# Kernel optimization log

Hardware: AMD Instinct MI355X
Metric: run time of the kernel (lower is better)

Reference implementation:

```python
import jax, jax.numpy as jnp
import numpy as np

N_H = 16
N_KV = 4
D_K = 128
ROPE_BASE = 10000.0


def _rope(t, cos, sin):
    # t: [B, T, H, d_k]; cos/sin: [1, T, 1, d_k//2]
    te, to = t[..., 0::2], t[..., 1::2]
    oe = te * cos - to * sin
    oo = te * sin + to * cos
    return jnp.stack([oe, oo], axis=-1).reshape(t.shape)


def setup_inputs() -> dict:
    key = jax.random.key(0)
    ks = jax.random.split(key, 5)
    B, T, d = 4, 2048, 2048
    s = 0.02
    return {
        "x": jax.random.normal(ks[0], (B, T, d), jnp.float32),
        "Wq": jax.random.normal(ks[1], (d, d), jnp.float32) * s,
        "Wk": jax.random.normal(ks[2], (d, N_KV * D_K), jnp.float32) * s,
        "Wv": jax.random.normal(ks[3], (d, N_KV * D_K), jnp.float32) * s,
        "Wp": jax.random.normal(ks[4], (d, d), jnp.float32) * s,
        "bp": jnp.zeros((d,), jnp.float32),
    }


def reference(x, Wq, Wk, Wv, Wp, bp):
    B, T, C = x.shape
    g = N_H // N_KV  # group size

    q = (x @ Wq).reshape(B, T, N_H, D_K)
    k = (x @ Wk).reshape(B, T, N_KV, D_K)
    v = (x @ Wv).reshape(B, T, N_KV, D_K)

    # RoPE frequencies (constants)
    theta = ROPE_BASE ** (-2.0 * jnp.arange(0, D_K, 2, dtype=jnp.float32) / D_K)
    freq = jnp.arange(T, dtype=jnp.float32)[:, None] * theta[None, :]  # [T, d_k//2]
    cos = jnp.cos(freq)[None, :, None, :]
    sin = jnp.sin(freq)[None, :, None, :]
    q = _rope(q, cos, sin)
    k = _rope(k, cos, sin)

    # GQA: group q heads by shared kv head (equiv to repeat_interleave on kv)
    q = q.reshape(B, T, N_KV, g, D_K).transpose(0, 2, 3, 1, 4)  # [B,n_kv,g,T,d_k]
    k = k.transpose(0, 2, 1, 3)  # [B,n_kv,T,d_k]
    v = v.transpose(0, 2, 1, 3)

    scores = jnp.einsum('bngqd,bnkd->bngqk', q, k) * (D_K ** -0.5)
    causal = jnp.tril(jnp.ones((T, T), bool))
    scores = jnp.where(causal, scores, -jnp.inf)
    attn = jax.nn.softmax(scores, axis=-1)
    out = jnp.einsum('bngqk,bnkd->bngqd', attn, v)  # [B,n_kv,g,T,d_k]
    out = out.transpose(0, 3, 1, 2, 4).reshape(B, T, C)
    return out @ Wp + bp
```

## Files before the change

kernel.cpp:

```cpp
#include <hip/hip_runtime.h>
#include <hip/hip_bf16.h>
#include <math.h>

typedef __bf16 bf16_t;
typedef __bf16 bf16x8 __attribute__((ext_vector_type(8)));
typedef __bf16 bf16x4 __attribute__((ext_vector_type(4)));
typedef float f32x4 __attribute__((ext_vector_type(4)));
typedef float f32x16 __attribute__((ext_vector_type(16)));
typedef unsigned int u32;

#define MFMA16 __builtin_amdgcn_mfma_f32_16x16x32_bf16
#define MFMA32 __builtin_amdgcn_mfma_f32_32x32x16_bf16

static __device__ __forceinline__ u32 pkbf(float a, float b) {
  union { bf16_t h[2]; u32 u; } z;
  z.h[0] = (bf16_t)a; z.h[1] = (bf16_t)b;
  return z.u;
}

static __device__ __forceinline__ void gload16(const bf16_t* g, bf16_t* l) {
  __builtin_amdgcn_global_load_lds(
      (const __attribute__((address_space(1))) void*)g,
      (__attribute__((address_space(3))) void*)l, 16, 0, 0);
}

__global__ void k_f32_to_bf16(const float* __restrict__ in, bf16_t* __restrict__ out, long n) {
  long i = ((long)blockIdx.x * blockDim.x + threadIdx.x) * 4;
  long stride = (long)gridDim.x * blockDim.x * 4;
  for (; i < n; i += stride) {
    const float4 v = *(const float4*)(in + i);
    bf16x4 o; o[0] = (bf16_t)v.x; o[1] = (bf16_t)v.y; o[2] = (bf16_t)v.z; o[3] = (bf16_t)v.w;
    *(bf16x4*)(out + i) = o;
  }
}

__global__ void k_transpose_bf16(const float* __restrict__ W, bf16_t* __restrict__ WT,
                                 int K, int N) {
  __shared__ float tile[32][33];
  int n0 = blockIdx.x * 32, k0 = blockIdx.y * 32;
  int tx = threadIdx.x & 31, ty = threadIdx.x >> 5;
#pragma unroll
  for (int i = 0; i < 4; i++)
    tile[ty + i * 8][tx] = W[(size_t)(k0 + ty + i * 8) * N + n0 + tx];
  __syncthreads();
#pragma unroll
  for (int i = 0; i < 4; i++) {
    int n = ty + i * 8;
    WT[(size_t)(n0 + n) * K + k0 + tx] = (bf16_t)tile[tx][n];
  }
}

__global__ void k_build_vt(const bf16_t* __restrict__ qkv, bf16_t* __restrict__ VT) {
  __shared__ bf16_t tile[32][33];
  int t0 = blockIdx.x * 32, c0 = blockIdx.y * 32, b = blockIdx.z;
  int tx = threadIdx.x & 31, ty = threadIdx.x >> 5;
  const bf16_t* src = qkv + (size_t)b * 2048 * 3072 + 2560;
#pragma unroll
  for (int i = 0; i < 4; i++)
    tile[ty + i * 8][tx] = src[(size_t)(t0 + ty + i * 8) * 3072 + c0 + tx];
  __syncthreads();
  bf16_t* dst = VT + (size_t)b * 512 * 2048;
#pragma unroll
  for (int i = 0; i < 4; i++)
    dst[(size_t)(c0 + ty + i * 8) * 2048 + t0 + tx] = tile[tx][ty + i * 8];
}

__global__ void k_rope(bf16_t* __restrict__ qkv) {
  int idx = blockIdx.x * blockDim.x + threadIdx.x;
  if (idx >= 8192 * 1280) return;
  int r = idx / 1280, p = idx - r * 1280;
  int t = r & 2047;
  int i = p & 63;
  float theta = exp2f(-(float)i * 0.41524101186092029f);
  float f = (float)t * theta;
  float s, c;
  sincosf(f, &s, &c);
  bf16_t* a = qkv + (size_t)r * 3072 + p * 2;
  float e = (float)a[0], o = (float)a[1];
  a[0] = (bf16_t)(e * c - o * s);
  a[1] = (bf16_t)(e * s + o * c);
}

template <bool F32OUT>
__global__ __launch_bounds__(256, 3) void k_gemm_bt(
    const bf16_t* __restrict__ A, const bf16_t* __restrict__ BT,
    bf16_t* __restrict__ Cb, float* __restrict__ Cf,
    const float* __restrict__ bias, int M, int N, int K, int nwg) {
  __shared__ bf16_t sA[128 * 64];
  __shared__ bf16_t sB[128 * 64];
  int nbn = N >> 7;
  int orig = (int)blockIdx.x;
  int swz = (orig & 7) * (nwg >> 3) + (orig >> 3);
  int bm = swz / nbn, bn = swz % nbn;
  int tid = threadIdx.x;
  int lane = tid & 63, wid = tid >> 6;
  int wm = (wid >> 1) << 6, wn = (wid & 1) << 6;
  int lr = lane & 15, lq = lane >> 4;
  f32x4 acc[4][4] = {};

  int srow = wid * 32 + (lane >> 3);
  int scol = (lane & 7) * 8;
  const bf16_t* Ag = A + (size_t)(bm * 128 + srow) * K + scol;
  const bf16_t* Bg = BT + (size_t)(bn * 128 + srow) * K + scol;
  bf16_t* Al = &sA[(wid * 32) * 64];
  bf16_t* Bl = &sB[(wid * 32) * 64];

  for (int k0 = 0; k0 < K; k0 += 64) {
#pragma unroll
    for (int i = 0; i < 4; i++) {
      gload16(Ag + (size_t)i * 8 * K + k0, Al + i * 8 * 64);
      gload16(Bg + (size_t)i * 8 * K + k0, Bl + i * 8 * 64);
    }
    __syncthreads();
#pragma unroll
    for (int kc = 0; kc < 2; kc++) {
      bf16x8 af[4], bfr[4];
#pragma unroll
      for (int m = 0; m < 4; m++)
        af[m] = *(const bf16x8*)&sA[(wm + m * 16 + lr) * 64 + kc * 32 + lq * 8];
#pragma unroll
      for (int n = 0; n < 4; n++)
        bfr[n] = *(const bf16x8*)&sB[(wn + n * 16 + lr) * 64 + kc * 32 + lq * 8];
#pragma unroll
      for (int m = 0; m < 4; m++)
#pragma unroll
        for (int n = 0; n < 4; n++)
          acc[m][n] = MFMA16(af[m], bfr[n], acc[m][n], 0, 0, 0);
    }
    __syncthreads();
  }
#pragma unroll
  for (int m = 0; m < 4; m++) {
    int row0 = bm * 128 + wm + m * 16 + lq * 4;
#pragma unroll
    for (int n = 0; n < 4; n++) {
      int col = bn * 128 + wn + n * 16 + lr;
#pragma unroll
      for (int r = 0; r < 4; r++) {
        if constexpr (F32OUT)
          Cf[(size_t)(row0 + r) * N + col] = acc[m][n][r] + bias[col];
        else
          Cb[(size_t)(row0 + r) * N + col] = (bf16_t)acc[m][n][r];
      }
    }
  }
}

__global__ __launch_bounds__(256, 2) void k_attn(const bf16_t* __restrict__ qkv,
                                                 const bf16_t* __restrict__ VT,
                                                 bf16_t* __restrict__ out) {
  __shared__ bf16_t sK[64 * 128];
  __shared__ bf16_t sVT[128 * 64];
  int bid = blockIdx.x;
  int g = bid >> 6;
  int qt = (g & 1) ? (g >> 1) : (15 - (g >> 1));
  int bh = bid & 63;
  int h = bh & 15, b = bh >> 4;
  int kvh = h >> 2;
  const size_t RS = 3072;
  const bf16_t* Qb = qkv + (size_t)b * 2048 * RS + h * 128;
  const bf16_t* Kb = qkv + (size_t)b * 2048 * RS + 2048 + kvh * 128;
  const bf16_t* Vt = VT + (size_t)(b * 4 + kvh) * 128 * 2048;
  int q0 = qt * 128;
  int tid = threadIdx.x, lane = tid & 63, wid = tid >> 6;
  int l31 = lane & 31, hi = lane >> 5;
  int qw = q0 + wid * 32;

  bf16x8 qf[8];
  {
    const bf16_t* qrow = Qb + (size_t)(qw + l31) * RS + hi * 8;
#pragma unroll
    for (int dc = 0; dc < 8; dc++)
      qf[dc] = *(const bf16x8*)(qrow + dc * 16);
  }

  f32x16 oT[4] = {};
  float m_r = -INFINITY, l_r = 0.f;
  const float SC = 0.08838834764831845f * 1.4426950408889634f;

  int k_row = tid >> 4, k_seg = tid & 15;
  int vd = tid >> 3, vk = (tid & 7) * 8;

  bf16x8 kreg[4], vreg[4];
  auto issue = [&](int k0) {
#pragma unroll
    for (int ps = 0; ps < 4; ps++)
      kreg[ps] = *(const bf16x8*)(Kb + (size_t)(k0 + k_row + ps * 16) * RS + k_seg * 8);
#pragma unroll
    for (int ps = 0; ps < 4; ps++)
      vreg[ps] = *(const bf16x8*)(Vt + (size_t)(vd + ps * 32) * 2048 + k0 + vk);
  };

  int ntiles = 2 * qt + 2;
  issue(0);
  for (int kt = 0; kt < ntiles; kt++) {
    int k0 = kt * 64;
#pragma unroll
    for (int ps = 0; ps < 4; ps++) {
      int row = k_row + ps * 16;
      int off = row * 256 + ((k_seg * 16) ^ ((row & 7) << 4));
      *(bf16x8*)((char*)sK + off) = kreg[ps];
    }
#pragma unroll
    for (int ps = 0; ps < 4; ps++) {
      int d = vd + ps * 32;
      int off = d * 128 + ((vk * 2) ^ ((d & 7) << 4));
      *(bf16x8*)((char*)sVT + off) = vreg[ps];
    }
    __syncthreads();
    if (kt + 1 < ntiles) issue(k0 + 64);

    if (k0 <= qw + 31) {
      f32x16 sa0 = {}, sa1 = {};
      __builtin_amdgcn_s_setprio(1);
#pragma unroll
      for (int dc = 0; dc < 8; dc++) {
        int cb = (dc * 32 + hi * 16) ^ ((l31 & 7) << 4);
        bf16x8 kf0 = *(const bf16x8*)((const char*)sK + l31 * 256 + cb);
        bf16x8 kf1 = *(const bf16x8*)((const char*)sK + (32 + l31) * 256 + cb);
        sa0 = MFMA32(kf0, qf[dc], sa0, 0, 0, 0);
        sa1 = MFMA32(kf1, qf[dc], sa1, 0, 0, 0);
      }
      __builtin_amdgcn_s_setprio(0);
      float p[2][16];
      int qg = qw + l31;
      if (k0 + 63 <= qw) {
#pragma unroll
        for (int r = 0; r < 16; r++) { p[0][r] = sa0[r]; p[1][r] = sa1[r]; }
      } else {
#pragma unroll
        for (int nf = 0; nf < 2; nf++)
#pragma unroll
          for (int r = 0; r < 16; r++) {
            int kg = k0 + nf * 32 + (r & 3) + 8 * (r >> 2) + 4 * hi;
            p[nf][r] = (kg <= qg) ? (nf ? sa1[r] : sa0[r]) : -INFINITY;
          }
      }
      float mx[16];
#pragma unroll
      for (int r = 0; r < 16; r++) mx[r] = fmaxf(p[0][r], p[1][r]);
#pragma unroll
      for (int s = 8; s >= 1; s >>= 1)
#pragma unroll
        for (int r = 0; r < 8; r++)
          if (r < s) mx[r] = fmaxf(mx[r], mx[r + s]);
      float pm = mx[0] * SC;
      pm = fmaxf(pm, __shfl_xor(pm, 32));
      bool skip = __all(pm <= m_r + 8.f);
      float mn = skip ? m_r : fmaxf(m_r, pm);
      float alpha = skip ? 1.f : exp2f(m_r - mn);
      m_r = mn;
      float nm = -m_r;
#pragma unroll
      for (int nf = 0; nf < 2; nf++)
#pragma unroll
        for (int r = 0; r < 16; r++)
          p[nf][r] = exp2f(fmaf(p[nf][r], SC, nm));
      float sm[16];
#pragma unroll
      for (int r = 0; r < 16; r++) sm[r] = p[0][r] + p[1][r];
#pragma unroll
      for (int s = 8; s >= 1; s >>= 1)
#pragma unroll
        for (int r = 0; r < 8; r++)
          if (r < s) sm[r] += sm[r + s];
      float rs = sm[0] + __shfl_xor(sm[0], 32);
      l_r = l_r * alpha + rs;
      if (!skip) {
#pragma unroll
        for (int c = 0; c < 4; c++)
#pragma unroll
          for (int r = 0; r < 16; r++) oT[c][r] *= alpha;
      }
#pragma unroll
      for (int nf = 0; nf < 2; nf++) {
        u32 Qk[4][2];
#pragma unroll
        for (int gg = 0; gg < 4; gg++) {
          Qk[gg][0] = pkbf(p[nf][4 * gg + 0], p[nf][4 * gg + 1]);
          Qk[gg][1] = pkbf(p[nf][4 * gg + 2], p[nf][4 * gg + 3]);
        }
#pragma unroll
        for (int kc = 0; kc < 2; kc++) {
          u32 x0 = __shfl_xor(Qk[2 * kc + 1 - hi][0], 32);
          u32 x1 = __shfl_xor(Qk[2 * kc + 1 - hi][1], 32);
          u32 o0 = Qk[2 * kc + hi][0], o1 = Qk[2 * kc + hi][1];
          union { u32 w[4]; bf16x8 v; } pf;
          pf.w[0] = hi ? x0 : o0;
          pf.w[1] = hi ? x1 : o1;
          pf.w[2] = hi ? o0 : x0;
          pf.w[3] = hi ? o1 : x1;
          int slot = nf * 2 + kc;
          int vb = (slot * 32 + hi * 16) ^ ((l31 & 7) << 4);
          __builtin_amdgcn_s_setprio(1);
#pragma unroll
          for (int c = 0; c < 4; c++) {
            bf16x8 vf = *(const bf16x8*)((const char*)sVT + (c * 32 + l31) * 128 + vb);
            oT[c] = MFMA32(vf, pf.v, oT[c], 0, 0, 0);
          }
          __builtin_amdgcn_s_setprio(0);
        }
      }
    }
    __syncthreads();
  }
  float inv = 1.f / l_r;
  size_t row = (size_t)b * 2048 + qw + l31;
#pragma unroll
  for (int c = 0; c < 4; c++)
#pragma unroll
    for (int rr = 0; rr < 4; rr++) {
      bf16x4 o4;
#pragma unroll
      for (int j = 0; j < 4; j++) o4[j] = (bf16_t)(oT[c][rr * 4 + j] * inv);
      *(bf16x4*)(out + row * 2048 + h * 128 + c * 32 + rr * 8 + hi * 4) = o4;
    }
}

extern "C" void kernel_launch(void* const* d_in, const int* in_sizes, int n_in,
                              void* d_out, int out_size, void* d_ws, size_t ws_size,
                              hipStream_t stream) {
  const float* x = (const float*)d_in[0];
  const float* Wq = (const float*)d_in[1];
  const float* Wk = (const float*)d_in[2];
  const float* Wv = (const float*)d_in[3];
  const float* Wp = (const float*)d_in[4];
  const float* bp = (const float*)d_in[5];
  float* out = (float*)d_out;

  bf16_t* ws = (bf16_t*)d_ws;
  bf16_t* xb = ws;
  bf16_t* qkv = ws + 16777216;
  bf16_t* WqkvT = ws + 16777216 + 25165824;
  bf16_t* WpT = WqkvT + 6291456;
  bf16_t* VT = WqkvT;

  k_f32_to_bf16<<<2048, 256, 0, stream>>>(x, xb, 16777216L);
  k_transpose_bf16<<<dim3(64, 64), 256, 0, stream>>>(Wq, WqkvT, 2048, 2048);
  k_transpose_bf16<<<dim3(16, 64), 256, 0, stream>>>(Wk, WqkvT + (size_t)2048 * 2048, 2048, 512);
  k_transpose_bf16<<<dim3(16, 64), 256, 0, stream>>>(Wv, WqkvT + (size_t)2560 * 2048, 2048, 512);
  k_transpose_bf16<<<dim3(64, 64), 256, 0, stream>>>(Wp, WpT, 2048, 2048);

  k_gemm_bt<false><<<64 * 24, 256, 0, stream>>>(xb, WqkvT, qkv, nullptr, nullptr, 8192, 3072, 2048, 64 * 24);
  k_rope<<<40960, 256, 0, stream>>>(qkv);
  k_build_vt<<<dim3(64, 16, 4), 256, 0, stream>>>(qkv, VT);
  k_attn<<<1024, 256, 0, stream>>>(qkv, VT, xb);
  k_gemm_bt<true><<<64 * 16, 256, 0, stream>>>(xb, WpT, nullptr, out, bp, 8192, 2048, 2048, 64 * 16);
}
```

Before: 435.8 us.

## Rewrite GEMM as 256x256 double-buffered swizzled tiles, pad attention V-transpose LDS

```diff
diff --git a/kernel.cpp b/kernel.cpp
--- a/kernel.cpp
+++ b/kernel.cpp
@@ -82,59 +82,123 @@
 }
 
 template <bool F32OUT>
-__global__ __launch_bounds__(256, 3) void k_gemm_bt(
+__global__ __launch_bounds__(512, 2) void k_gemm_bt(
     const bf16_t* __restrict__ A, const bf16_t* __restrict__ BT,
     bf16_t* __restrict__ Cb, float* __restrict__ Cf,
     const float* __restrict__ bias, int M, int N, int K, int nwg) {
-  __shared__ bf16_t sA[128 * 64];
-  __shared__ bf16_t sB[128 * 64];
-  int nbn = N >> 7;
+  __shared__ bf16_t smem[65536];
+  const int nbn = N >> 8;
   int orig = (int)blockIdx.x;
   int swz = (orig & 7) * (nwg >> 3) + (orig >> 3);
   int bm = swz / nbn, bn = swz % nbn;
-  int tid = threadIdx.x;
-  int lane = tid & 63, wid = tid >> 6;
-  int wm = (wid >> 1) << 6, wn = (wid & 1) << 6;
-  int lr = lane & 15, lq = lane >> 4;
-  f32x4 acc[4][4] = {};
-
-  int srow = wid * 32 + (lane >> 3);
-  int scol = (lane & 7) * 8;
-  const bf16_t* Ag = A + (size_t)(bm * 128 + srow) * K + scol;
-  const bf16_t* Bg = BT + (size_t)(bn * 128 + srow) * K + scol;
-  bf16_t* Al = &sA[(wid * 32) * 64];
-  bf16_t* Bl = &sB[(wid * 32) * 64];
-
-  for (int k0 = 0; k0 < K; k0 += 64) {
+  const int tid = threadIdx.x;
+  const int lane = tid & 63, wid = tid >> 6;
+  const int wm = (wid >> 2) << 7;
+  const int wn = (wid & 3) << 6;
+  const int lr = lane & 15, lq = lane >> 4;
+  f32x4 acc[8][4] = {};
+
+  const int rl = tid >> 3;
+  const int ss = (tid & 7) ^ (rl & 7);
+  const bf16_t* gA = A + (size_t)(bm * 256 + rl) * K + ss * 8;
+  const bf16_t* gB = BT + (size_t)(bn * 256 + rl) * K + ss * 8;
+  const int lo = wid * 512;
+
+  const int nt = K >> 6;
+  {
+    bf16_t* sA0 = smem;
+    bf16_t* sB0 = smem + 16384;
 #pragma unroll
     for (int i = 0; i < 4; i++) {
-      gload16(Ag + (size_t)i * 8 * K + k0, Al + i * 8 * 64);
-      gload16(Bg + (size_t)i * 8 * K + k0, Bl + i * 8 * 64);
-    }
-    __syncthreads();
-#pragma unroll
-    for (int kc = 0; kc < 2; kc++) {
-      bf16x8 af[4], bfr[4];
-#pragma unroll
-      for (int m = 0; m < 4; m++)
-        af[m] = *(const bf16x8*)&sA[(wm + m * 16 + lr) * 64 + kc * 32 + lq * 8];
-#pragma unroll
-      for (int n = 0; n < 4; n++)
-        bfr[n] = *(const bf16x8*)&sB[(wn + n * 16 + lr) * 64 + kc * 32 + lq * 8];
-#pragma unroll
-      for (int m = 0; m < 4; m++)
+      gload16(gA + (size_t)i * 64 * K, sA0 + i * 4096 + lo);
+      gload16(gB + (size_t)i * 64 * K, sB0 + i * 4096 + lo);
+    }
+  }
+  asm volatile("s_waitcnt vmcnt(0)" ::: "memory");
+  __syncthreads();
+
+  for (int t = 0; t < nt; ++t) {
+    bf16_t* sAc = smem + (t & 1) * 32768;
+    bf16_t* sBc = sAc + 16384;
+    bf16_t* sAn = smem + ((t & 1) ^ 1) * 32768;
+    bf16_t* sBn = sAn + 16384;
+    const int k1 = (t + 1) << 6;
+    bf16x8 breg[4][2];
+#pragma unroll
+    for (int n = 0; n < 4; n++)
+#pragma unroll
+      for (int kk = 0; kk < 2; kk++) {
+        int R = wn + n * 16 + lr;
+        int u = (kk * 4 + lq) ^ (R & 7);
+        breg[n][kk] = *(const bf16x8*)&sBc[R * 64 + u * 8];
+      }
+    {
+      bf16x8 areg[2][2];
+#pragma unroll
+      for (int ml = 0; ml < 2; ml++)
+#pragma unroll
+        for (int kk = 0; kk < 2; kk++) {
+          int R = wm + ml * 16 + lr;
+          int u = (kk * 4 + lq) ^ (R & 7);
+          areg[ml][kk] = *(const bf16x8*)&sAc[R * 64 + u * 8];
+        }
+      if (t + 1 < nt) {
+#pragma unroll
+        for (int i = 0; i < 4; i++) {
+          gload16(gA + (size_t)i * 64 * K + k1, sAn + i * 4096 + lo);
+          gload16(gB + (size_t)i * 64 * K + k1, sBn + i * 4096 + lo);
+        }
+      }
+      __builtin_amdgcn_s_barrier();
+      asm volatile("s_waitcnt lgkmcnt(0)" ::: "memory");
+      __builtin_amdgcn_sched_barrier(0);
+      __builtin_amdgcn_s_setprio(1);
+#pragma unroll
+      for (int ml = 0; ml < 2; ml++)
 #pragma unroll
         for (int n = 0; n < 4; n++)
-          acc[m][n] = MFMA16(af[m], bfr[n], acc[m][n], 0, 0, 0);
-    }
-    __syncthreads();
-  }
-#pragma unroll
-  for (int m = 0; m < 4; m++) {
-    int row0 = bm * 128 + wm + m * 16 + lq * 4;
+#pragma unroll
+          for (int kk = 0; kk < 2; kk++)
+            acc[ml][n] = MFMA16(areg[ml][kk], breg[n][kk], acc[ml][n], 0, 0, 0);
+      __builtin_amdgcn_s_setprio(0);
+      __builtin_amdgcn_s_barrier();
+    }
+#pragma unroll
+    for (int p = 1; p < 4; p++) {
+      bf16x8 areg[2][2];
+#pragma unroll
+      for (int ml = 0; ml < 2; ml++)
+#pragma unroll
+        for (int kk = 0; kk < 2; kk++) {
+          int R = wm + (2 * p + ml) * 16 + lr;
+          int u = (kk * 4 + lq) ^ (R & 7);
+          areg[ml][kk] = *(const bf16x8*)&sAc[R * 64 + u * 8];
+        }
+      __builtin_amdgcn_s_barrier();
+      asm volatile("s_waitcnt lgkmcnt(0)" ::: "memory");
+      __builtin_amdgcn_sched_barrier(0);
+      __builtin_amdgcn_s_setprio(1);
+#pragma unroll
+      for (int ml = 0; ml < 2; ml++)
+#pragma unroll
+        for (int n = 0; n < 4; n++)
+#pragma unroll
+          for (int kk = 0; kk < 2; kk++)
+            acc[2 * p + ml][n] = MFMA16(areg[ml][kk], breg[n][kk], acc[2 * p + ml][n], 0, 0, 0);
+      __builtin_amdgcn_s_setprio(0);
+      if (p == 3) {
+        asm volatile("s_waitcnt vmcnt(0)" ::: "memory");
+        __builtin_amdgcn_sched_barrier(0);
+      }
+      __builtin_amdgcn_s_barrier();
+    }
+  }
+#pragma unroll
+  for (int m = 0; m < 8; m++) {
+    int row0 = bm * 256 + wm + m * 16 + lq * 4;
 #pragma unroll
     for (int n = 0; n < 4; n++) {
-      int col = bn * 128 + wn + n * 16 + lr;
+      int col = bn * 256 + wn + n * 16 + lr;
 #pragma unroll
       for (int r = 0; r < 4; r++) {
         if constexpr (F32OUT)
@@ -150,7 +214,7 @@
                                                  const bf16_t* __restrict__ VT,
                                                  bf16_t* __restrict__ out) {
   __shared__ bf16_t sK[64 * 128];
-  __shared__ bf16_t sVT[128 * 64];
+  __shared__ bf16_t sVT[128 * 72];
   int bid = blockIdx.x;
   int g = bid >> 6;
   int qt = (g & 1) ? (g >> 1) : (15 - (g >> 1));
@@ -202,11 +266,8 @@
       *(bf16x8*)((char*)sK + off) = kreg[ps];
     }
 #pragma unroll
-    for (int ps = 0; ps < 4; ps++) {
-      int d = vd + ps * 32;
-      int off = d * 128 + ((vk * 2) ^ ((d & 7) << 4));
-      *(bf16x8*)((char*)sVT + off) = vreg[ps];
-    }
+    for (int ps = 0; ps < 4; ps++)
+      *(bf16x8*)&sVT[(vd + ps * 32) * 72 + vk] = vreg[ps];
     __syncthreads();
     if (kt + 1 < ntiles) issue(k0 + 64);
 
@@ -291,11 +352,10 @@
           pf.w[2] = hi ? o0 : x0;
           pf.w[3] = hi ? o1 : x1;
           int slot = nf * 2 + kc;
-          int vb = (slot * 32 + hi * 16) ^ ((l31 & 7) << 4);
           __builtin_amdgcn_s_setprio(1);
 #pragma unroll
           for (int c = 0; c < 4; c++) {
-            bf16x8 vf = *(const bf16x8*)((const char*)sVT + (c * 32 + l31) * 128 + vb);
+            bf16x8 vf = *(const bf16x8*)&sVT[(c * 32 + l31) * 72 + slot * 16 + hi * 8];
             oT[c] = MFMA32(vf, pf.v, oT[c], 0, 0, 0);
           }
           __builtin_amdgcn_s_setprio(0);
@@ -341,9 +401,9 @@
   k_transpose_bf16<<<dim3(16, 64), 256, 0, stream>>>(Wv, WqkvT + (size_t)2560 * 2048, 2048, 512);
   k_transpose_bf16<<<dim3(64, 64), 256, 0, stream>>>(Wp, WpT, 2048, 2048);
 
-  k_gemm_bt<false><<<64 * 24, 256, 0, stream>>>(xb, WqkvT, qkv, nullptr, nullptr, 8192, 3072, 2048, 64 * 24);
+  k_gemm_bt<false><<<384, 512, 0, stream>>>(xb, WqkvT, qkv, nullptr, nullptr, 8192, 3072, 2048, 384);
   k_rope<<<40960, 256, 0, stream>>>(qkv);
   k_build_vt<<<dim3(64, 16, 4), 256, 0, stream>>>(qkv, VT);
   k_attn<<<1024, 256, 0, stream>>>(qkv, VT, xb);
-  k_gemm_bt<true><<<64 * 16, 256, 0, stream>>>(xb, WpT, nullptr, out, bp, 8192, 2048, 2048, 64 * 16);
-}
+  k_gemm_bt<true><<<256, 512, 0, stream>>>(xb, WpT, nullptr, out, bp, 8192, 2048, 2048, 256);
+}
```

New measurement: 389.1 us. 1.12x faster.
